# Kernel tuning notes

Measured on AMD Instinct MI355X. Metric: run time of the kernel, lower is better.

Reference implementation:

```python
import jax, jax.numpy as jnp
import numpy as np

MUL0, MUL1 = 64, 32          # 64x0e + 32x1e irreps_emb
D_FEAT = MUL0 + 3 * MUL1     # 160
N_T, N_Q, N_K = 64, 1024, 1024


def quat_apply(q, v):
    # q: (...,4) real-first (w,x,y,z); v: (...,3). Rotate v by q.
    w = q[..., :1]
    u = q[..., 1:]
    uv = jnp.cross(u, v)
    return v + 2.0 * (w * uv + jnp.cross(u, uv))


def split_irreps(f):
    # f: (..., 160) -> scalars (...,64), vectors (...,32,3)
    s = f[..., :MUL0]
    v = f[..., MUL0:].reshape(f.shape[:-1] + (MUL1, 3))
    return s, v


def dtp(a, b, Ws, Wv):
    # Depthwise tensor product restricted to l<=1 (SeparableFCTP analogue),
    # output irreps 1x0e + 32x1e, with SiLU activation on the scalar part.
    sa, va = split_irreps(a)
    sb, vb = split_irreps(b)
    # scalar paths: 0e*0e and 1e.1e (dot) -> 96 scalar channels
    scal = jnp.concatenate([sa * sb, jnp.einsum('...ci,...ci->...c', va, vb)], axis=-1)
    # vector paths: 0e*1e, 1e*0e, 1e x 1e (cross) -> 96 vector channels
    vec = jnp.concatenate(
        [sa[..., :MUL1, None] * vb, va * sb[..., :MUL1, None], jnp.cross(va, vb)], axis=-2)
    out_s = jax.nn.silu(scal @ Ws)                    # (...,1)
    out_v = jnp.einsum('...ci,co->...oi', vec, Wv)    # (...,32,3)
    return out_s, out_v


def get_key_features(points, key_coord, key_feat, W_key):
    # radius-style key lookup: nearest key node + smooth radial envelope + linear
    d2 = jnp.sum((points[:, None, :] - key_coord[None, :, :]) ** 2, axis=-1)  # (M, N_K)
    idx = jnp.argmin(d2, axis=-1)
    dist = jnp.sqrt(jnp.take_along_axis(d2, idx[:, None], axis=1)[:, 0])
    env = jnp.exp(-dist)[:, None]
    return (key_feat[idx] * env) @ W_key              # (M, 160)


def setup_inputs() -> dict:
    key = jax.random.key(0)
    ks = jax.random.split(key, 11)
    return {
        'T': jax.random.normal(ks[0], (N_T, 7), jnp.float32),
        'query_weight': jax.random.uniform(ks[1], (N_Q,), jnp.float32),
        'query_feature': jax.random.normal(ks[2], (N_Q, D_FEAT), jnp.float32),
        'query_coord': jax.random.normal(ks[3], (N_Q, 3), jnp.float32),
        'key_coord': jax.random.normal(ks[4], (N_K, 3), jnp.float32),
        'key_node_feature': jax.random.normal(ks[5], (N_K, D_FEAT), jnp.float32),
        'W_key': jax.random.normal(ks[6], (D_FEAT, D_FEAT), jnp.float32) / np.sqrt(D_FEAT),
        'Ws_lin': jax.random.normal(ks[7], (96, 1), jnp.float32) / np.sqrt(96.0),
        'Wv_lin': jax.random.normal(ks[8], (96, 32), jnp.float32) / np.sqrt(96.0),
        'Ws_ang': jax.random.normal(ks[9], (96, 1), jnp.float32) / np.sqrt(96.0),
        'Wv_ang': jax.random.normal(ks[10], (96, 32), jnp.float32) / np.sqrt(96.0),
    }


def reference(T, query_weight, query_feature, query_coord, key_coord,
              key_node_feature, W_key, Ws_lin, Wv_lin, Ws_ang, Wv_ang):
    n_t = T.shape[0]
    n_q = query_feature.shape[0]
    q = T[:, :4]
    q = q / jnp.linalg.norm(q, axis=-1, keepdims=True)
    X = T[:, 4:]
    # transform query coords by each pose: (N_T, N_Q, 3)
    qc_t = quat_apply(q[:, None, :], query_coord[None, :, :]) + X[:, None, :]
    # equivariant feature transform: scalars unchanged, vectors rotated
    s, v = split_irreps(query_feature)
    v_t = quat_apply(q[:, None, None, :], v[None])                    # (N_T,N_Q,32,3)
    qf_t = jnp.concatenate(
        [jnp.broadcast_to(s, (n_t,) + s.shape), v_t.reshape(n_t, n_q, 3 * MUL1)],
        axis=-1).reshape(n_t * n_q, D_FEAT)
    # key feature gather over the expanded N_T*N_Q batch
    kf = get_key_features(qc_t.reshape(-1, 3), key_coord, key_node_feature, W_key)
    # two tensor products; original drops leading scalar ([..., 1:])
    _, lin = dtp(qf_t, kf, Ws_lin, Wv_lin)
    _, ang = dtp(qf_t, kf, Ws_ang, Wv_ang)
    lin = lin.reshape(n_t, n_q, MUL1, 3).mean(axis=-2)
    ang = ang.reshape(n_t, n_q, MUL1, 3).mean(axis=-2)
    # rotate back into body frame
    qinv = q * jnp.array([1.0, -1.0, -1.0, -1.0], q.dtype)
    lin = quat_apply(qinv[:, None, :], lin)
    ang = quat_apply(qinv[:, None, :], ang)
    ang_orbital = jnp.cross(query_coord[None], lin)
    lin_vel = jnp.einsum('q,tqi->ti', query_weight, lin)
    ang_vel = jnp.einsum('q,tqi->ti', query_weight, ang_orbital + ang)
    return lin_vel, ang_vel
```

## Files before the change

### kernel.cpp

```cpp
#include <hip/hip_runtime.h>
#include <math.h>

#define NT 64
#define NQ 1024
#define NK 1024
#define WS_KW 0
#define WS_QF 131072
#define WS_WV 262144
#define WS_KP 262400

__launch_bounds__(256)
__global__ void prep_kernel(const float* __restrict__ qfeat,
                            const float* __restrict__ keyfeat,
                            const float* __restrict__ Wkey,
                            const float* __restrict__ WvL,
                            const float* __restrict__ WvA,
                            const float* __restrict__ kcoord,
                            float* __restrict__ ws,
                            float* __restrict__ out) {
  const int blk = blockIdx.x;
  const int tid = threadIdx.x;
  if (blk < 128) {
    const int g = blk * 256 + tid;
    const int r = g >> 5;
    const int c = g & 31;
    const float* kf = keyfeat + r * 160;
    const int c0 = 64 + 3 * c;
    float a0 = 0.f, a1 = 0.f, a2 = 0.f, a3 = 0.f;
#pragma unroll 4
    for (int k = 0; k < 160; ++k) {
      const float f = kf[k];
      const float* wr = Wkey + k * 160;
      a0 = fmaf(f, wr[c0 + 0], a0);
      a1 = fmaf(f, wr[c0 + 1], a1);
      a2 = fmaf(f, wr[c0 + 2], a2);
      a3 = fmaf(f, wr[c], a3);
    }
    reinterpret_cast<float4*>(ws + WS_KW)[g] = make_float4(a0, a1, a2, a3);
  } else if (blk < 256) {
    const int g = (blk - 128) * 256 + tid;
    const int p = g >> 5;
    const int c = g & 31;
    const float* q = qfeat + p * 160;
    float4 o = make_float4(q[64 + 3 * c], q[65 + 3 * c], q[66 + 3 * c], q[c]);
    reinterpret_cast<float4*>(ws + WS_QF)[c * 1024 + p] = o;
  } else {
    out[tid] = 0.f;
    if (tid < 128) out[256 + tid] = 0.f;
    float4* kp = reinterpret_cast<float4*>(ws + WS_KP);
#pragma unroll
    for (int j = 0; j < 4; ++j) {
      const int k = j * 256 + tid;
      kp[k] = make_float4(kcoord[k * 3 + 0], kcoord[k * 3 + 1], kcoord[k * 3 + 2], 0.f);
    }
    if (tid < 32) {
      const int c = tid;
      float m0 = 0.f, m1 = 0.f, m2 = 0.f, m3 = 0.f, m4 = 0.f, m5 = 0.f;
      for (int o = 0; o < 32; ++o) {
        m0 += WvL[c * 32 + o];
        m1 += WvL[(32 + c) * 32 + o];
        m2 += WvL[(64 + c) * 32 + o];
        m3 += WvA[c * 32 + o];
        m4 += WvA[(32 + c) * 32 + o];
        m5 += WvA[(64 + c) * 32 + o];
      }
      float* wv = ws + WS_WV + c * 8;
      const float s = 1.0f / 32.0f;
      wv[0] = m0 * s; wv[1] = m1 * s; wv[2] = m2 * s;
      wv[3] = m3 * s; wv[4] = m4 * s; wv[5] = m5 * s;
      wv[6] = 0.f; wv[7] = 0.f;
    }
  }
}

__launch_bounds__(256)
__global__ void main_kernel(const float* __restrict__ T,
                            const float* __restrict__ qweight,
                            const float* __restrict__ qcoord,
                            const float* __restrict__ ws,
                            float* __restrict__ out) {
  __shared__ float4 keys[1024];
  __shared__ float2 cand[4][128];
  __shared__ float red[4][8];
  const int tid  = threadIdx.x;
  const int lane = tid & 63;
  const int wu   = __builtin_amdgcn_readfirstlane(tid >> 6);
  const int t    = blockIdx.x >> 3;
  const int pg   = blockIdx.x & 7;

  {
    const float4* kp = reinterpret_cast<const float4*>(ws + WS_KP);
#pragma unroll
    for (int j = 0; j < 4; ++j) keys[j * 256 + tid] = kp[j * 256 + tid];
  }

  const float* Tt = T + t * 7;
  float qw = Tt[0], qx = Tt[1], qy = Tt[2], qz = Tt[3];
  const float Xx = Tt[4], Xy = Tt[5], Xz = Tt[6];
  const float rn = rsqrtf(qw * qw + qx * qx + qy * qy + qz * qz);
  qw *= rn; qx *= rn; qy *= rn; qz *= rn;
  const float ix = -qx, iy = -qy, iz = -qz;

  const int qA = pg * 128 + lane;
  const int qB = qA + 64;
  const float qax = qcoord[qA * 3 + 0], qay = qcoord[qA * 3 + 1], qaz = qcoord[qA * 3 + 2];
  const float qbx = qcoord[qB * 3 + 0], qby = qcoord[qB * 3 + 1], qbz = qcoord[qB * 3 + 2];
  const float uax = qy * qaz - qz * qay, uay = qz * qax - qx * qaz, uaz = qx * qay - qy * qax;
  const float qcax = qax + 2.0f * (qw * uax + (qy * uaz - qz * uay)) + Xx;
  const float qcay = qay + 2.0f * (qw * uay + (qz * uax - qx * uaz)) + Xy;
  const float qcaz = qaz + 2.0f * (qw * uaz + (qx * uay - qy * uax)) + Xz;
  const float ubx = qy * qbz - qz * qby, uby = qz * qbx - qx * qbz, ubz = qx * qby - qy * qbx;
  const float qcbx = qbx + 2.0f * (qw * ubx + (qy * ubz - qz * uby)) + Xx;
  const float qcby = qby + 2.0f * (qw * uby + (qz * ubx - qx * ubz)) + Xy;
  const float qcbz = qbz + 2.0f * (qw * ubz + (qx * uby - qy * ubx)) + Xz;

  __syncthreads();

  const int kbase = wu * 256;
  float mvA = 1e30f, mvB = 1e30f;
  int miA = 0, miB = 0;
#pragma unroll 8
  for (int m = 0; m < 256; ++m) {
    const float4 K = keys[kbase + m];
    const float dax = qcax - K.x, day = qcay - K.y, daz = qcaz - K.z;
    const float dbx = qcbx - K.x, dby = qcby - K.y, dbz = qcbz - K.z;
    const float dA = dax * dax + day * day + daz * daz;
    const float dB = dbx * dbx + dby * dby + dbz * dbz;
    if (dA < mvA) { mvA = dA; miA = kbase + m; }
    if (dB < mvB) { mvB = dB; miB = kbase + m; }
  }
  cand[wu][lane]      = make_float2(mvA, __int_as_float(miA));
  cand[wu][64 + lane] = make_float2(mvB, __int_as_float(miB));
  __syncthreads();

  const int pl  = tid >> 1;
  const int sub = tid & 1;
  const float2 ca = cand[2 * sub][pl];
  const float2 cb = cand[2 * sub + 1][pl];
  float mv = ca.x; int mi = __float_as_int(ca.y);
  {
    const float vb2 = cb.x; const int ib2 = __float_as_int(cb.y);
    if (vb2 < mv || (vb2 == mv && ib2 < mi)) { mv = vb2; mi = ib2; }
  }
  {
    const float vo = __shfl_xor(mv, 1);
    const int   io = __shfl_xor(mi, 1);
    if (vo < mv || (vo == mv && io < mi)) { mv = vo; mi = io; }
  }
  const int minidx = mi;
  const float env = expf(-sqrtf(mv));

  const int pF = pg * 128 + pl;
  const float qpx = qcoord[pF * 3 + 0];
  const float qpy = qcoord[pF * 3 + 1];
  const float qpz = qcoord[pF * 3 + 2];

  const float4* kwrow = reinterpret_cast<const float4*>(ws + WS_KW) + minidx * 32;
  const float4* qfp   = reinterpret_cast<const float4*>(ws + WS_QF) + pF;
  const float* wv = ws + WS_WV;
  float lx = 0.f, ly = 0.f, lz = 0.f, ax = 0.f, ay = 0.f, az = 0.f;
#pragma unroll
  for (int jj = 0; jj < 16; ++jj) {
    const int c = 2 * jj + sub;
    const float4 B = kwrow[c];
    const float4 A = qfp[c * 1024];
    const float uvx = iy * B.z - iz * B.y;
    const float uvy = iz * B.x - ix * B.z;
    const float uvz = ix * B.y - iy * B.x;
    const float bx = B.x + 2.0f * (qw * uvx + (iy * uvz - iz * uvy));
    const float by = B.y + 2.0f * (qw * uvy + (iz * uvx - ix * uvz));
    const float bz = B.z + 2.0f * (qw * uvz + (ix * uvy - iy * uvx));
    const float crx = A.y * bz - A.z * by;
    const float cry = A.z * bx - A.x * bz;
    const float crz = A.x * by - A.y * bx;
    const float* w6 = wv + c * 8;
    const float a1L = w6[0] * A.w, a2L = w6[1] * B.w, w3L = w6[2];
    const float a1A = w6[3] * A.w, a2A = w6[4] * B.w, w3A = w6[5];
    lx = fmaf(a1L, bx, fmaf(a2L, A.x, fmaf(w3L, crx, lx)));
    ly = fmaf(a1L, by, fmaf(a2L, A.y, fmaf(w3L, cry, ly)));
    lz = fmaf(a1L, bz, fmaf(a2L, A.z, fmaf(w3L, crz, lz)));
    ax = fmaf(a1A, bx, fmaf(a2A, A.x, fmaf(w3A, crx, ax)));
    ay = fmaf(a1A, by, fmaf(a2A, A.y, fmaf(w3A, cry, ay)));
    az = fmaf(a1A, bz, fmaf(a2A, A.z, fmaf(w3A, crz, az)));
  }
  lx += __shfl_xor(lx, 1); ly += __shfl_xor(ly, 1); lz += __shfl_xor(lz, 1);
  ax += __shfl_xor(ax, 1); ay += __shfl_xor(ay, 1); az += __shfl_xor(az, 1);
  lx *= env; ly *= env; lz *= env;
  ax *= env; ay *= env; az *= env;

  const float wp = qweight[pF];
  const float ox = qpy * lz - qpz * ly;
  const float oy = qpz * lx - qpx * lz;
  const float oz = qpx * ly - qpy * lx;
  float r0 = wp * lx, r1 = wp * ly, r2 = wp * lz;
  float r3 = wp * (ox + ax), r4 = wp * (oy + ay), r5 = wp * (oz + az);

#pragma unroll
  for (int m = 32; m >= 1; m >>= 1) {
    r0 += __shfl_xor(r0, m);
    r1 += __shfl_xor(r1, m);
    r2 += __shfl_xor(r2, m);
    r3 += __shfl_xor(r3, m);
    r4 += __shfl_xor(r4, m);
    r5 += __shfl_xor(r5, m);
  }
  if (lane == 0) {
    red[wu][0] = r0; red[wu][1] = r1; red[wu][2] = r2;
    red[wu][3] = r3; red[wu][4] = r4; red[wu][5] = r5;
  }
  __syncthreads();
  if (tid < 6) {
    const float s = red[0][tid] + red[1][tid] + red[2][tid] + red[3][tid];
    const int row = (tid < 3) ? (t * 3 + tid) : (192 + t * 3 + (tid - 3));
    atomicAdd(out + row, s * 0.5f);
  }
}

extern "C" void kernel_launch(void* const* d_in, const int* in_sizes, int n_in,
                              void* d_out, int out_size, void* d_ws, size_t ws_size,
                              hipStream_t stream) {
  const float* T   = (const float*)d_in[0];
  const float* qw  = (const float*)d_in[1];
  const float* qf  = (const float*)d_in[2];
  const float* qc  = (const float*)d_in[3];
  const float* kc  = (const float*)d_in[4];
  const float* kf  = (const float*)d_in[5];
  const float* Wk  = (const float*)d_in[6];
  const float* WvL = (const float*)d_in[8];
  const float* WvA = (const float*)d_in[10];
  float* out = (float*)d_out;
  float* ws  = (float*)d_ws;

  prep_kernel<<<257, 256, 0, stream>>>(qf, kf, Wk, WvL, WvA, kc, ws, out);
  main_kernel<<<512, 256, 0, stream>>>(T, qw, qc, ws, out);
}
```

Baseline: 107.1 us.

## Double block size and register-tile four queries per thread in nearest-key search

Main kernel now uses 512-thread blocks covering 256 queries each, halving the grid and the number of times the 1024-key table is staged into shared memory. In the argmin loop each thread keeps four query points in registers and eight waves each scan 128 keys, so every shared-memory key load is reused across four distance computations. The cost is more registers per thread and a larger candidate reduction; halving the grid to 256 blocks on a large GPU may lower occupancy and load balance.

```diff
diff --git a/kernel.cpp b/kernel.cpp
--- a/kernel.cpp
+++ b/kernel.cpp
@@ -73,25 +73,25 @@
   }
 }
 
-__launch_bounds__(256)
+__launch_bounds__(512)
 __global__ void main_kernel(const float* __restrict__ T,
                             const float* __restrict__ qweight,
                             const float* __restrict__ qcoord,
                             const float* __restrict__ ws,
                             float* __restrict__ out) {
   __shared__ float4 keys[1024];
-  __shared__ float2 cand[4][128];
-  __shared__ float red[4][8];
+  __shared__ float2 cand[8][256];
+  __shared__ float red[8][8];
   const int tid  = threadIdx.x;
   const int lane = tid & 63;
   const int wu   = __builtin_amdgcn_readfirstlane(tid >> 6);
-  const int t    = blockIdx.x >> 3;
-  const int pg   = blockIdx.x & 7;
+  const int t    = blockIdx.x >> 2;
+  const int pg   = blockIdx.x & 3;
 
   {
     const float4* kp = reinterpret_cast<const float4*>(ws + WS_KP);
-#pragma unroll
-    for (int j = 0; j < 4; ++j) keys[j * 256 + tid] = kp[j * 256 + tid];
+    keys[tid]       = kp[tid];
+    keys[512 + tid] = kp[512 + tid];
   }
 
   const float* Tt = T + t * 7;
@@ -101,48 +101,61 @@
   qw *= rn; qx *= rn; qy *= rn; qz *= rn;
   const float ix = -qx, iy = -qy, iz = -qz;
 
-  const int qA = pg * 128 + lane;
-  const int qB = qA + 64;
-  const float qax = qcoord[qA * 3 + 0], qay = qcoord[qA * 3 + 1], qaz = qcoord[qA * 3 + 2];
-  const float qbx = qcoord[qB * 3 + 0], qby = qcoord[qB * 3 + 1], qbz = qcoord[qB * 3 + 2];
-  const float uax = qy * qaz - qz * qay, uay = qz * qax - qx * qaz, uaz = qx * qay - qy * qax;
-  const float qcax = qax + 2.0f * (qw * uax + (qy * uaz - qz * uay)) + Xx;
-  const float qcay = qay + 2.0f * (qw * uay + (qz * uax - qx * uaz)) + Xy;
-  const float qcaz = qaz + 2.0f * (qw * uaz + (qx * uay - qy * uax)) + Xz;
-  const float ubx = qy * qbz - qz * qby, uby = qz * qbx - qx * qbz, ubz = qx * qby - qy * qbx;
-  const float qcbx = qbx + 2.0f * (qw * ubx + (qy * ubz - qz * uby)) + Xx;
-  const float qcby = qby + 2.0f * (qw * uby + (qz * ubx - qx * ubz)) + Xy;
-  const float qcbz = qbz + 2.0f * (qw * ubz + (qx * uby - qy * ubx)) + Xz;
+  float qcx[4], qcy[4], qcz[4];
+#pragma unroll
+  for (int j = 0; j < 4; ++j) {
+    const int q = pg * 256 + j * 64 + lane;
+    const float px = qcoord[q * 3 + 0];
+    const float py = qcoord[q * 3 + 1];
+    const float pz = qcoord[q * 3 + 2];
+    const float ux = qy * pz - qz * py;
+    const float uy = qz * px - qx * pz;
+    const float uz = qx * py - qy * px;
+    qcx[j] = px + 2.0f * (qw * ux + (qy * uz - qz * uy)) + Xx;
+    qcy[j] = py + 2.0f * (qw * uy + (qz * ux - qx * uz)) + Xy;
+    qcz[j] = pz + 2.0f * (qw * uz + (qx * uy - qy * ux)) + Xz;
+  }
 
   __syncthreads();
 
-  const int kbase = wu * 256;
-  float mvA = 1e30f, mvB = 1e30f;
-  int miA = 0, miB = 0;
-#pragma unroll 8
-  for (int m = 0; m < 256; ++m) {
+  const int kbase = wu * 128;
+  float mv0 = 1e30f, mv1 = 1e30f, mv2 = 1e30f, mv3 = 1e30f;
+  int mi0 = 0, mi1 = 0, mi2 = 0, mi3 = 0;
+#pragma unroll 4
+  for (int m = 0; m < 128; ++m) {
     const float4 K = keys[kbase + m];
-    const float dax = qcax - K.x, day = qcay - K.y, daz = qcaz - K.z;
-    const float dbx = qcbx - K.x, dby = qcby - K.y, dbz = qcbz - K.z;
-    const float dA = dax * dax + day * day + daz * daz;
-    const float dB = dbx * dbx + dby * dby + dbz * dbz;
-    if (dA < mvA) { mvA = dA; miA = kbase + m; }
-    if (dB < mvB) { mvB = dB; miB = kbase + m; }
-  }
-  cand[wu][lane]      = make_float2(mvA, __int_as_float(miA));
-  cand[wu][64 + lane] = make_float2(mvB, __int_as_float(miB));
+    const float d0x = qcx[0] - K.x, d0y = qcy[0] - K.y, d0z = qcz[0] - K.z;
+    const float d1x = qcx[1] - K.x, d1y = qcy[1] - K.y, d1z = qcz[1] - K.z;
+    const float d2x = qcx[2] - K.x, d2y = qcy[2] - K.y, d2z = qcz[2] - K.z;
+    const float d3x = qcx[3] - K.x, d3y = qcy[3] - K.y, d3z = qcz[3] - K.z;
+    const float d0 = d0x * d0x + d0y * d0y + d0z * d0z;
+    const float d1 = d1x * d1x + d1y * d1y + d1z * d1z;
+    const float d2 = d2x * d2x + d2y * d2y + d2z * d2z;
+    const float d3 = d3x * d3x + d3y * d3y + d3z * d3z;
+    const int ki = kbase + m;
+    if (d0 < mv0) { mv0 = d0; mi0 = ki; }
+    if (d1 < mv1) { mv1 = d1; mi1 = ki; }
+    if (d2 < mv2) { mv2 = d2; mi2 = ki; }
+    if (d3 < mv3) { mv3 = d3; mi3 = ki; }
+  }
+  cand[wu][0 * 64 + lane] = make_float2(mv0, __int_as_float(mi0));
+  cand[wu][1 * 64 + lane] = make_float2(mv1, __int_as_float(mi1));
+  cand[wu][2 * 64 + lane] = make_float2(mv2, __int_as_float(mi2));
+  cand[wu][3 * 64 + lane] = make_float2(mv3, __int_as_float(mi3));
   __syncthreads();
 
   const int pl  = tid >> 1;
   const int sub = tid & 1;
-  const float2 ca = cand[2 * sub][pl];
-  const float2 cb = cand[2 * sub + 1][pl];
-  float mv = ca.x; int mi = __float_as_int(ca.y);
+  float mv; int mi;
   {
-    const float vb2 = cb.x; const int ib2 = __float_as_int(cb.y);
-    if (vb2 < mv || (vb2 == mv && ib2 < mi)) { mv = vb2; mi = ib2; }
-  }
-  {
+    const float2 c0 = cand[4 * sub][pl];
+    mv = c0.x; mi = __float_as_int(c0.y);
+#pragma unroll
+    for (int i = 1; i < 4; ++i) {
+      const float2 ci = cand[4 * sub + i][pl];
+      const float vi = ci.x; const int ii = __float_as_int(ci.y);
+      if (vi < mv || (vi == mv && ii < mi)) { mv = vi; mi = ii; }
+    }
     const float vo = __shfl_xor(mv, 1);
     const int   io = __shfl_xor(mi, 1);
     if (vo < mv || (vo == mv && io < mi)) { mv = vo; mi = io; }
@@ -150,7 +163,7 @@
   const int minidx = mi;
   const float env = expf(-sqrtf(mv));
 
-  const int pF = pg * 128 + pl;
+  const int pF = pg * 256 + pl;
   const float qpx = qcoord[pF * 3 + 0];
   const float qpy = qcoord[pF * 3 + 1];
   const float qpz = qcoord[pF * 3 + 2];
@@ -210,7 +223,9 @@
   }
   __syncthreads();
   if (tid < 6) {
-    const float s = red[0][tid] + red[1][tid] + red[2][tid] + red[3][tid];
+    float s = 0.f;
+#pragma unroll
+    for (int w = 0; w < 8; ++w) s += red[w][tid];
     const int row = (tid < 3) ? (t * 3 + tid) : (192 + t * 3 + (tid - 3));
     atomicAdd(out + row, s * 0.5f);
   }
@@ -232,5 +247,5 @@
   float* ws  = (float*)d_ws;
 
   prep_kernel<<<257, 256, 0, stream>>>(qf, kf, Wk, WvL, WvA, kc, ws, out);
-  main_kernel<<<512, 256, 0, stream>>>(T, qw, qc, ws, out);
+  main_kernel<<<256, 512, 0, stream>>>(T, qw, qc, ws, out);
 }
```

New measurement: 109.1 us. No clear change (+1.9%).
